# Kernel optimization log

Hardware: AMD Instinct MI355X
Metric: run time of the kernel (lower is better)

The kernel has to match this reference:

```python
import jax, jax.numpy as jnp
import numpy as np

B, T, D, H = 2, 4096, 1024, 16
DK, DV, C = 64, 128, 64  # head_k_dim, head_v_dim, chunk size


def setup_inputs() -> dict:
    key = jax.random.key(0)
    ks = jax.random.split(key, 7)
    std = 0.02
    return {
        "x": jax.random.normal(ks[0], (B, T, D), jnp.float32),
        "Wq": jax.random.normal(ks[1], (D, D), jnp.float32) * std,
        "Wk": jax.random.normal(ks[2], (D, D), jnp.float32) * std,
        "Wv": jax.random.normal(ks[3], (D, 2 * D), jnp.float32) * std,
        "Wg": jax.random.normal(ks[4], (D, 2 * D), jnp.float32) * std,
        "Wo": jax.random.normal(ks[5], (2 * D, D), jnp.float32) * std,
        "g_norm_w": jnp.ones((DV,), jnp.float32),
    }


def _rope(q, k):  # q,k: [B,T,H,DK], neox-style rotate-half rotary
    dk = q.shape[-1]
    inv = 1.0 / (10000.0 ** (jnp.arange(0, dk, 2, dtype=jnp.float32) / dk))
    t = jnp.arange(q.shape[1], dtype=jnp.float32)
    f = t[:, None] * inv[None, :]                      # [T, dk/2]
    cos = jnp.cos(f)[None, :, None, :]
    sin = jnp.sin(f)[None, :, None, :]
    def rot(x):
        x1, x2 = jnp.split(x, 2, axis=-1)
        return jnp.concatenate([x1 * cos - x2 * sin, x1 * sin + x2 * cos], -1)
    return rot(q), rot(k)


def reference(x, Wq, Wk, Wv, Wg, Wo, g_norm_w):
    b, t, _ = x.shape
    nc = t // C
    q = (x @ Wq).reshape(b, t, H, DK)
    k = (x @ Wk).reshape(b, t, H, DK)
    v = (x @ Wv).reshape(b, t, H, DV)
    g = (x @ Wg).reshape(b, t, H, DV)
    q, k = _rope(q, k)
    q = q * (DK ** -0.5)

    # per-head retention decay: gamma_h = 1 - 2^(-5-h)
    gamma = 1.0 - jnp.exp2(-5.0 - jnp.arange(H, dtype=jnp.float32))  # [H]
    i = jnp.arange(C, dtype=jnp.float32)
    dq = gamma[:, None] ** (i + 1.0)          # [H,C] cross-chunk decay on q
    dkv = gamma[:, None] ** (C - 1.0 - i)     # [H,C] decay of k into state
    rel = i[:, None] - i[None, :]
    Dmat = jnp.where(rel >= 0, gamma[:, None, None] ** jnp.maximum(rel, 0.0), 0.0)  # [H,C,C]
    gC = gamma ** C

    to_chunks = lambda a: a.reshape(b, nc, C, H, a.shape[-1]).transpose(1, 0, 3, 2, 4)
    qc, kc, vc = to_chunks(q), to_chunks(k), to_chunks(v)  # [NC,B,H,C,d]

    def step(S, inp):
        qi, ki, vi = inp
        o_inter = jnp.einsum('bhcd,bhde->bhce', qi * dq[None, :, :, None], S)
        A = jnp.einsum('bhid,bhjd->bhij', qi, ki) * Dmat[None]
        o_intra = jnp.einsum('bhij,bhje->bhie', A, vi)
        S = gC[None, :, None, None] * S + jnp.einsum('bhjd,bhje->bhde', ki * dkv[None, :, :, None], vi)
        return S, o_inter + o_intra

    S0 = jnp.zeros((b, H, DK, DV), x.dtype)
    _, o = jax.lax.scan(step, S0, (qc, kc, vc))            # [NC,B,H,C,DV]
    o = o.transpose(1, 0, 3, 2, 4).reshape(b, t, H, DV)

    # fused per-head RMSNorm + swish gate
    rms = o * jax.lax.rsqrt(jnp.mean(o * o, axis=-1, keepdims=True) + 1e-5) * g_norm_w
    o = rms * (g * jax.nn.sigmoid(g))
    return o.reshape(b, t, H * DV) @ Wo
```

## Files before the change

kernel.cpp:

```cpp
#include <hip/hip_runtime.h>
#include <stdint.h>
#include <type_traits>

typedef unsigned short u16;
typedef __attribute__((ext_vector_type(8))) short short8;
typedef __attribute__((ext_vector_type(4))) float f32x4;

#define MFMA16(a,b,c) __builtin_amdgcn_mfma_f32_16x16x32_bf16(a,b,c,0,0,0)

__device__ __forceinline__ u16 f2bf(float f){
  uint32_t u = __builtin_bit_cast(uint32_t, f);
  u += 0x7FFFu + ((u>>16)&1u);
  return (u16)(u>>16);
}
__device__ __forceinline__ float bf2f(u16 h){
  uint32_t u = ((uint32_t)h)<<16;
  return __builtin_bit_cast(float, u);
}

__global__ __launch_bounds__(256) void prep(const float* __restrict__ x, u16* __restrict__ xb,
    const float* __restrict__ Wq, const float* __restrict__ Wk, const float* __restrict__ Wv,
    const float* __restrict__ Wg, const float* __restrict__ Wo,
    u16* __restrict__ WcatT, u16* __restrict__ WoT){
  int bid = blockIdx.x;
  if (bid < 8192){
    int i = (bid*256 + threadIdx.x)*4;
    float4 v = *(const float4*)&x[i];
    uint2 u;
    u.x = (uint32_t)f2bf(v.x) | ((uint32_t)f2bf(v.y)<<16);
    u.y = (uint32_t)f2bf(v.z) | ((uint32_t)f2bf(v.w)<<16);
    *(uint2*)&xb[i] = u;
    return;
  }
  bid -= 8192;
  const float* src; u16* dst; int R, Cc, tc, tr;
  if (bid < 1024){        src=Wq; dst=WcatT;             R=1024; Cc=1024; int b=bid;      tc=(b&31)*32; tr=(b>>5)*32; }
  else if (bid < 2048){   src=Wk; dst=WcatT+1024*1024;   R=1024; Cc=1024; int b=bid-1024; tc=(b&31)*32; tr=(b>>5)*32; }
  else if (bid < 4096){   src=Wv; dst=WcatT+2048*1024;   R=1024; Cc=2048; int b=bid-2048; tc=(b&63)*32; tr=(b>>6)*32; }
  else if (bid < 6144){   src=Wg; dst=WcatT+4096*1024;   R=1024; Cc=2048; int b=bid-4096; tc=(b&63)*32; tr=(b>>6)*32; }
  else {                  src=Wo; dst=WoT;               R=2048; Cc=1024; int b=bid-6144; tc=(b&31)*32; tr=(b>>5)*32; }
  __shared__ float tile[32][33];
  int lr = threadIdx.x>>5, lc = threadIdx.x&31;
  #pragma unroll
  for (int p=0;p<4;p++)
    tile[lr+p*8][lc] = src[(size_t)(tr+lr+p*8)*Cc + tc + lc];
  __syncthreads();
  #pragma unroll
  for (int p=0;p<4;p++)
    dst[(size_t)(tc+lr+p*8)*R + tr + lc] = f2bf(tile[lc][lr+p*8]);
}

__global__ __launch_bounds__(512,1) void gemm1_256(const u16* __restrict__ A,
    const u16* __restrict__ BT, u16* __restrict__ C){
  __shared__ u16 L[4*16384];
  const int flat = blockIdx.y*24 + blockIdx.x;
  const int xcd  = flat & 7, loc = flat >> 3;
  const int bm   = xcd*4 + (loc & 3);
  const int bn   = loc >> 2;
  const int t = threadIdx.x;
  const int w = t>>6, l = t&63;
  const int wm = w>>2, wn = w&3;
  const int lr = l&15, lg = l>>4;
  const int srow = t>>2;
  const int gsw = ((t&3) - (t>>3)) & 3;
  const size_t aoff = (size_t)(bm*256 + srow)*1024 + gsw*8;
  const size_t boff = (size_t)(bn*256 + srow)*1024 + gsw*8;
  const int sdo = t*8;

  u16 *p0 = L, *p1 = L+16384, *p2 = L+32768, *p3 = L+49152;

  auto STAGE = [&](u16* buf, int k0){
    __builtin_amdgcn_global_load_lds(&A[aoff + k0],                     buf + sdo,               16,0,0);
    __builtin_amdgcn_global_load_lds(&A[aoff + (size_t)128*1024 + k0],  buf + sdo + 4096,        16,0,0);
    __builtin_amdgcn_global_load_lds(&BT[boff + k0],                    buf + 8192 + sdo,        16,0,0);
    __builtin_amdgcn_global_load_lds(&BT[boff + (size_t)128*1024 + k0], buf + 8192 + sdo + 4096, 16,0,0);
  };
  auto LDA = [&](const u16* base, int row)->short8 {
    return *(const short8*)(base + row*32 + (((lg + (row>>1))&3)<<3));
  };

  f32x4 acc[8][4];
  #pragma unroll
  for (int m=0;m<8;m++)
    #pragma unroll
    for (int n=0;n<4;n++) acc[m][n] = (f32x4){0.f,0.f,0.f,0.f};

  STAGE(p0, 0); STAGE(p1, 32); STAGE(p2, 64);
  asm volatile("s_waitcnt vmcnt(8)" ::: "memory");
  __builtin_amdgcn_s_barrier();
  short8 afA[4], afB[4], bf4[4], bf4n[4];
  #pragma unroll
  for (int m=0;m<4;m++) afA[m] = LDA(p0, wm*128 + m*16 + lr);
  #pragma unroll
  for (int n=0;n<4;n++) bf4[n] = LDA(p0 + 8192, wn*64 + n*16 + lr);

  for (int kt=0; kt<32; ++kt){
    #pragma unroll
    for (int m=0;m<4;m++) afB[m] = LDA(p0, wm*128 + (m+4)*16 + lr);
    if (kt+3 < 32) STAGE(p3, (kt+3)*32);
    __builtin_amdgcn_s_setprio(1);
    #pragma unroll
    for (int m=0;m<4;m++)
      #pragma unroll
      for (int n=0;n<4;n++)
        acc[m][n] = MFMA16(afA[m], bf4[n], acc[m][n]);
    __builtin_amdgcn_s_setprio(0);
    asm volatile("s_waitcnt lgkmcnt(0)" ::: "memory");
    __builtin_amdgcn_sched_barrier(0);
    if      (kt < 29)  asm volatile("s_waitcnt vmcnt(8)" ::: "memory");
    else if (kt == 29) asm volatile("s_waitcnt vmcnt(4)" ::: "memory");
    else               asm volatile("s_waitcnt vmcnt(0)" ::: "memory");
    __builtin_amdgcn_s_barrier();
    __builtin_amdgcn_sched_barrier(0);
    if (kt+1 < 32){
      #pragma unroll
      for (int m=0;m<4;m++) afA[m]  = LDA(p1, wm*128 + m*16 + lr);
      #pragma unroll
      for (int n=0;n<4;n++) bf4n[n] = LDA(p1 + 8192, wn*64 + n*16 + lr);
    }
    __builtin_amdgcn_s_setprio(1);
    #pragma unroll
    for (int m=0;m<4;m++)
      #pragma unroll
      for (int n=0;n<4;n++)
        acc[m+4][n] = MFMA16(afB[m], bf4[n], acc[m+4][n]);
    __builtin_amdgcn_s_setprio(0);
    if (kt+1 < 32){
      #pragma unroll
      for (int n=0;n<4;n++) bf4[n] = bf4n[n];
    }
    { u16* tp=p0; p0=p1; p1=p2; p2=p3; p3=tp; }
  }

  __syncthreads();
  const bool qk = (bn < 8);
  const float qscale = (bn < 4) ? 0.125f : 1.0f;
  #pragma unroll
  for (int s=0;s<4;++s){
    if (wm == (s>>1)){
      #pragma unroll
      for (int mm=0;mm<4;++mm){
        const int m = (s&1)*4 + mm;
        if (qk){
          #pragma unroll
          for (int n=0;n<2;n++){
            float inv = exp2f((float)(n*16+lr) * (-13.287712379549449f/32.0f));
            #pragma unroll
            for (int r=0;r<4;r++){
              int grow = bm*256 + wm*128 + m*16 + lg*4 + r;
              float f = (float)(grow & 4095) * inv;
              float sn, cs; __sincosf(f, &sn, &cs);
              float x1 = acc[m][n][r], x2 = acc[m][n+2][r];
              int lrow = mm*16 + lg*4 + r;
              L[lrow*264 + wn*64 + n*16 + lr]     = f2bf((x1*cs - x2*sn)*qscale);
              L[lrow*264 + wn*64 + (n+2)*16 + lr] = f2bf((x1*sn + x2*cs)*qscale);
            }
          }
        } else {
          #pragma unroll
          for (int n=0;n<4;n++)
            #pragma unroll
            for (int r=0;r<4;r++)
              L[(mm*16+lg*4+r)*264 + wn*64 + n*16 + lr] = f2bf(acc[m][n][r]);
        }
      }
    }
    __syncthreads();
    #pragma unroll
    for (int p=0;p<4;p++){
      int idx = p*512 + t;
      int row = idx>>5, gr = idx&31;
      *(short8*)&C[(size_t)(bm*256 + s*64 + row)*6144 + bn*256 + gr*8] =
        *(const short8*)&L[row*264 + gr*8];
    }
    __syncthreads();
  }
}

__global__ __launch_bounds__(256) void gemm2_nt(const u16* __restrict__ A,
    const u16* __restrict__ BT, float* __restrict__ C, int M, int N, int K){
  __shared__ u16 L[3*8192];
  const int flat = blockIdx.y*gridDim.x + blockIdx.x;
  const int xcd  = flat & 7, loc = flat >> 3;
  const int bm   = xcd*8 + (loc & 7);
  const int bn   = loc >> 3;
  const int t = threadIdx.x;
  const int w = t>>6, l = t&63;
  const int wr = (w>>1)*64, wc = (w&1)*64;
  const int lr = l&15, lg = l>>4;
  const int srow = t>>2;
  const int gsw  = ((t&3) - (t>>3)) & 3;
  const int scol = gsw*8;
  const size_t aoff = (size_t)(bm*128 + srow)*K + scol;
  const size_t boff = (size_t)(bn*128 + srow)*K + scol;
  const int sdo = t*8;

  u16 *a0 = L,          *b0 = L + 4096;
  u16 *a1 = L + 8192,   *b1 = L + 12288;
  u16 *a2 = L + 16384,  *b2 = L + 20480;

  auto STAGE = [&](u16* la, u16* lb, int k0){
    __builtin_amdgcn_global_load_lds(&A[aoff + k0],                 la + sdo,        16, 0, 0);
    __builtin_amdgcn_global_load_lds(&A[aoff + (size_t)64*K + k0],  la + sdo + 2048, 16, 0, 0);
    __builtin_amdgcn_global_load_lds(&BT[boff + k0],                lb + sdo,        16, 0, 0);
    __builtin_amdgcn_global_load_lds(&BT[boff + (size_t)64*K + k0], lb + sdo + 2048, 16, 0, 0);
  };
  auto LDR = [&](const u16* base, int row)->short8 {
    return *(const short8*)(base + row*32 + (((lg + (row>>1))&3)<<3));
  };

  f32x4 acc[4][4];
  for (int m=0;m<4;m++) for (int n=0;n<4;n++) acc[m][n] = (f32x4){0.f,0.f,0.f,0.f};

  const int NT = K >> 5;
  STAGE(a0, b0, 0);
  STAGE(a1, b1, 32);
  asm volatile("s_waitcnt vmcnt(4)" ::: "memory");
  __builtin_amdgcn_s_barrier();
  short8 af01[2], af23[2], bfr[4], bfrn[4];
  #pragma unroll
  for (int m=0;m<2;m++) af01[m] = LDR(a0, wr + m*16 + lr);
  #pragma unroll
  for (int n=0;n<4;n++) bfr[n] = LDR(b0, wc + n*16 + lr);

  for (int kt=0; kt<NT; ++kt){
    #pragma unroll
    for (int m=0;m<2;m++) af23[m] = LDR(a0, wr + (m+2)*16 + lr);
    if (kt+2 < NT) STAGE(a2, b2, (kt+2)*32);
    __builtin_amdgcn_s_setprio(1);
    #pragma unroll
    for (int m=0;m<2;m++)
      #pragma unroll
      for (int n=0;n<4;n++)
        acc[m][n] = MFMA16(af01[m], bfr[n], acc[m][n]);
    __builtin_amdgcn_s_setprio(0);
    asm volatile("s_waitcnt lgkmcnt(0)" ::: "memory");
    __builtin_amdgcn_sched_barrier(0);
    if (kt < NT-2) asm volatile("s_waitcnt vmcnt(4)" ::: "memory");
    else           asm volatile("s_waitcnt vmcnt(0)" ::: "memory");
    __builtin_amdgcn_s_barrier();
    __builtin_amdgcn_sched_barrier(0);
    if (kt+1 < NT){
      #pragma unroll
      for (int m=0;m<2;m++) af01[m] = LDR(a1, wr + m*16 + lr);
      #pragma unroll
      for (int n=0;n<4;n++) bfrn[n] = LDR(b1, wc + n*16 + lr);
    }
    __builtin_amdgcn_s_setprio(1);
    #pragma unroll
    for (int m=0;m<2;m++)
      #pragma unroll
      for (int n=0;n<4;n++)
        acc[m+2][n] = MFMA16(af23[m], bfr[n], acc[m+2][n]);
    __builtin_amdgcn_s_setprio(0);
    if (kt+1 < NT){
      #pragma unroll
      for (int n=0;n<4;n++) bfr[n] = bfrn[n];
    }
    { u16* tp=a0; a0=a1; a1=a2; a2=tp; }
    { u16* tp=b0; b0=b1; b1=b2; b2=tp; }
  }

  #pragma unroll
  for (int m=0;m<4;m++)
    #pragma unroll
    for (int n=0;n<4;n++){
    int row = bm*128 + wr + m*16 + lg*4;
    int col = bn*128 + wc + n*16 + lr;
    #pragma unroll
    for (int r=0;r<4;r++)
      C[(size_t)(row+r)*N + col] = acc[m][n][r];
  }
}

__global__ __launch_bounds__(256) void retention_r1(const u16* __restrict__ qkvg,
    u16* __restrict__ o, u16* __restrict__ states){
  int bid = blockIdx.x;
  int c = bid & 63, h = (bid>>6)&15, b = bid>>10;
  int t = threadIdx.x, w = t>>6, l = t&63, lr = l&15, lg = l>>4;
  __shared__ u16 SH[17280];
  __shared__ float pw[72];
  u16* kT    = SH;
  u16* vT    = SH + 4096;
  u16* A_lds = SH + 12288;
  float log2g = log2f(1.0f - exp2f(-5.0f - (float)h));
  if (t < 65) pw[t] = exp2f(log2g*(float)t);
  const size_t rowbase = (size_t)(b*4096 + c*64);
  __syncthreads();

  {
    int rp = t>>3, cg = t&7;
    int r0 = rp*2;
    short8 k0v = *(const short8*)&qkvg[(rowbase+r0  )*6144 + 1024 + h*64 + cg*8];
    short8 k1v = *(const short8*)&qkvg[(rowbase+r0+1)*6144 + 1024 + h*64 + cg*8];
    float d0 = pw[63-r0], d1 = pw[62-r0];
    #pragma unroll
    for (int j=0;j<8;j++){
      int d = cg*8+j;
      uint32_t pk = (uint32_t)f2bf(bf2f((u16)k0v[j])*d0) | ((uint32_t)f2bf(bf2f((u16)k1v[j])*d1)<<16);
      *(uint32_t*)&kT[d*64 + (((r0>>3) ^ (d>>3))<<3) + (r0&7)] = pk;
    }
    #pragma unroll
    for (int p=0;p<2;p++){
      int it = t + p*256;
      int vrp = it>>4, vcg = it&15;
      int vr0 = vrp*2;
      short8 v0 = *(const short8*)&qkvg[(rowbase+vr0  )*6144 + 2048 + h*128 + vcg*8];
      short8 v1 = *(const short8*)&qkvg[(rowbase+vr0+1)*6144 + 2048 + h*128 + vcg*8];
      #pragma unroll
      for (int j=0;j<8;j++){
        int e = vcg*8+j;
        uint32_t pv = (uint32_t)(u16)v0[j] | ((uint32_t)(u16)v1[j]<<16);
        *(uint32_t*)&vT[e*64 + (((vr0>>3) ^ ((e>>3)&7))<<3) + (vr0&7)] = pv;
      }
    }
  }

  f32x4 z4 = {0.f,0.f,0.f,0.f};
  f32x4 accA[4] = {z4,z4,z4,z4};
  #pragma unroll
  for (int ks=0;ks<2;ks++){
    short8 aq = *(const short8*)&qkvg[(rowbase + w*16+lr)*6144 + h*64 + ks*32 + lg*8];
    #pragma unroll
    for (int n=0;n<4;n++){
      short8 bk = *(const short8*)&qkvg[(rowbase + n*16+lr)*6144 + 1024 + h*64 + ks*32 + lg*8];
      accA[n] = MFMA16(aq, bk, accA[n]);
    }
  }
  #pragma unroll
  for (int n=0;n<4;n++)
    #pragma unroll
    for (int r=0;r<4;r++){
    int i = w*16 + lg*4 + r, j = n*16 + lr;
    float v = (i>=j) ? accA[n][r]*pw[i-j] : 0.0f;
    A_lds[i*72 + j] = f2bf(v);
  }
  __syncthreads();

  f32x4 accO[8], accS[8];
  #pragma unroll
  for (int n=0;n<8;n++){ accO[n]=z4; accS[n]=z4; }
  #pragma unroll
  for (int ks=0;ks<2;ks++){
    int rk = w*16+lr;
    short8 aA = *(const short8*)&A_lds[rk*72 + ks*32+lg*8];
    short8 aK = *(const short8*)&kT[rk*64 + (((ks*4+lg) ^ (rk>>3))<<3)];
    #pragma unroll
    for (int n=0;n<8;n++){
      int e2 = n*16+lr;
      short8 bv = *(const short8*)&vT[e2*64 + (((ks*4+lg) ^ ((e2>>3)&7))<<3)];
      accO[n] = MFMA16(aA, bv, accO[n]);
      accS[n] = MFMA16(aK, bv, accS[n]);
    }
  }

  __syncthreads();
  u16* oB = SH;
  u16* sB = SH + 8448;
  #pragma unroll
  for (int n=0;n<8;n++)
    #pragma unroll
    for (int r=0;r<4;r++){
    int i = w*16 + lg*4 + r, e = n*16 + lr;
    oB[i*132 + e] = f2bf(accO[n][r]);
    sB[e*68 + i]  = f2bf(accS[n][r]);
  }
  __syncthreads();
  const size_t ob = rowbase*2048 + h*128;
  const size_t sb = ((size_t)(b*16+h)*64 + c)*8192;
  {
    int orow = t>>2, ocol = (t&3)*32;
    #pragma unroll
    for (int q=0;q<4;q++)
      *(short8*)&o[ob + (size_t)orow*2048 + ocol + q*8] = *(const short8*)&oB[orow*132 + ocol + q*8];
    int se = t>>1, sd = (t&1)*32;
    #pragma unroll
    for (int q=0;q<4;q++)
      *(short8*)&states[sb + (size_t)se*64 + sd + q*8] = *(const short8*)&sB[se*68 + sd + q*8];
  }
}

__global__ __launch_bounds__(256) void retention_r2(const u16* __restrict__ qkvg,
    const u16* __restrict__ states, u16* __restrict__ o){
  int bid = blockIdx.x;
  int xq = bid & 7, qq = bid >> 3;
  int bh = xq*4 + (qq & 3);
  int vblk = qq >> 2;
  int h = bh & 15, b = bh >> 4;
  int t = threadIdx.x, w = t>>6, l = t&63, lr = l&15, lg = l>>4;
  int e0 = vblk*16;
  float log2g = log2f(1.0f - exp2f(-5.0f - (float)h));
  float gC = exp2f(64.0f*log2g);
  float dqv[4];
  #pragma unroll
  for (int r=0;r<4;r++) dqv[r] = exp2f(log2g*(float)(w*16 + lg*4 + r + 1));
  float st[16];
  #pragma unroll
  for (int i=0;i<16;i++) st[i]=0.f;
  const size_t sbase = ((size_t)(b*16+h)*64)*8192 + (size_t)(e0+lr)*64 + lg*8;
  const size_t qb = (size_t)(b*4096)*6144 + h*64 + (size_t)(w*16+lr)*6144 + lg*8;
  const size_t obh = (size_t)(b*4096)*2048 + h*128 + e0 + lr;
  short8 nsc0 = *(const short8*)&states[sbase];
  short8 nsc1 = *(const short8*)&states[sbase + 32];
  short8 naq0 = *(const short8*)&qkvg[qb];
  short8 naq1 = *(const short8*)&qkvg[qb + 32];
  for (int c=0;c<64;c++){
    short8 sc0 = nsc0, sc1 = nsc1, aq0 = naq0, aq1 = naq1;
    if (c < 63){
      nsc0 = *(const short8*)&states[sbase + (size_t)(c+1)*8192];
      nsc1 = *(const short8*)&states[sbase + (size_t)(c+1)*8192 + 32];
      naq0 = *(const short8*)&qkvg[qb + (size_t)(c+1)*64*6144];
      naq1 = *(const short8*)&qkvg[qb + (size_t)(c+1)*64*6144 + 32];
    }
    f32x4 acc = {0.f,0.f,0.f,0.f};
    short8 bs0, bs1;
    #pragma unroll
    for (int dd=0;dd<8;dd++) bs0[dd] = (short)f2bf(st[dd]);
    #pragma unroll
    for (int dd=0;dd<8;dd++) bs1[dd] = (short)f2bf(st[dd+8]);
    acc = MFMA16(aq0, bs0, acc);
    acc = MFMA16(aq1, bs1, acc);
    #pragma unroll
    for (int r=0;r<4;r++){
      int i = w*16 + lg*4 + r;
      size_t oi = obh + (size_t)(c*64 + i)*2048;
      o[oi] = f2bf(bf2f(o[oi]) + dqv[r]*acc[r]);
    }
    #pragma unroll
    for (int i2=0;i2<8;i2++) st[i2]   = gC*st[i2]   + bf2f((u16)sc0[i2]);
    #pragma unroll
    for (int i2=0;i2<8;i2++) st[i2+8] = gC*st[i2+8] + bf2f((u16)sc1[i2]);
  }
}

__global__ __launch_bounds__(256) void norm_gate(const u16* __restrict__ o,
    const u16* __restrict__ qkvg, const float* __restrict__ gnw, u16* __restrict__ og){
  int g16 = threadIdx.x >> 4;
  int l16 = threadIdx.x & 15;
  int rowh = blockIdx.x*16 + g16;
  int row = rowh >> 4, h = rowh & 15;
  short8 vv = *(const short8*)(o + (size_t)row*2048 + h*128 + l16*8);
  float v[8];
  float ss = 0.f;
  #pragma unroll
  for (int j=0;j<8;j++){ v[j] = bf2f((u16)vv[j]); ss += v[j]*v[j]; }
  #pragma unroll
  for (int off=8; off; off>>=1) ss += __shfl_xor(ss, off);
  float rs = rsqrtf(ss*(1.0f/128.0f) + 1e-5f);
  short8 gg = *(const short8*)(qkvg + (size_t)row*6144 + 4096 + h*128 + l16*8);
  float4 w0 = *(const float4*)&gnw[l16*8];
  float4 w1 = *(const float4*)&gnw[l16*8 + 4];
  float wv[8] = {w0.x,w0.y,w0.z,w0.w,w1.x,w1.y,w1.z,w1.w};
  short8 res;
  #pragma unroll
  for (int j=0;j<8;j++){
    float gj = bf2f((u16)gg[j]);
    float rj = v[j]*rs*wv[j] * (gj/(1.f+expf(-gj)));
    res[j] = (short)f2bf(rj);
  }
  *(short8*)(og + (size_t)row*2048 + h*128 + l16*8) = res;
}

extern "C" void kernel_launch(void* const* d_in, const int* in_sizes, int n_in,
                              void* d_out, int out_size, void* d_ws, size_t ws_size,
                              hipStream_t stream){
  const float* x   = (const float*)d_in[0];
  const float* Wq  = (const float*)d_in[1];
  const float* Wk  = (const float*)d_in[2];
  const float* Wv  = (const float*)d_in[3];
  const float* Wg  = (const float*)d_in[4];
  const float* Wo  = (const float*)d_in[5];
  const float* gnw = (const float*)d_in[6];
  float* out = (float*)d_out;

  const size_t NEED = 171966464ull;
  if (ws_size < NEED) return;

  char* base = (char*)d_ws;
  u16* qkvg  = (u16*)(base);
  u16* obuf  = (u16*)(base + 100663296);
  u16* WoT   = (u16*)(base + 134217728);
  u16* xb    = (u16*)(base + 138412032);
  u16* WcatT = (u16*)(base + 155189248);
  u16* stt   = (u16*)(base + 138412032);
  u16* og    = (u16*)(base + 138412032);

  prep<<<16384,256,0,stream>>>(x, xb, Wq, Wk, Wv, Wg, Wo, WcatT, WoT);
  gemm1_256<<<dim3(24,32),512,0,stream>>>(xb, WcatT, qkvg);
  retention_r1<<<2048,256,0,stream>>>(qkvg, obuf, stt);
  retention_r2<<<256,256,0,stream>>>(qkvg, stt, obuf);
  norm_gate<<<8192,256,0,stream>>>(obuf, qkvg, gnw, og);
  gemm2_nt<<<dim3(8,64),256,0,stream>>>(og, WoT, out, 8192, 1024, 2048);
}
```

Baseline: 283.2 us.

## Switch projection GEMM to double-buffered BK=64 stages with full-K fragment preload

Replaces the four-slot, one-barrier-per-32-K pipeline in the fused QKVG projection GEMM with two 64-wide K buffers. Each iteration loads fragments for both 32-K halves and issues one 64-K stage ahead. This halves the barrier and loop count and gives 32 MFMAs per half. In exchange, prefetch depth drops from three stages to one and the loop waits on vmcnt(0) every iteration, so global-load latency may be less hidden. Fragment register pressure also rises.

```diff
diff --git a/kernel.cpp b/kernel.cpp
--- a/kernel.cpp
+++ b/kernel.cpp
@@ -52,7 +52,7 @@
 
 __global__ __launch_bounds__(512,1) void gemm1_256(const u16* __restrict__ A,
     const u16* __restrict__ BT, u16* __restrict__ C){
-  __shared__ u16 L[4*16384];
+  __shared__ u16 L[2*32768];
   const int flat = blockIdx.y*24 + blockIdx.x;
   const int xcd  = flat & 7, loc = flat >> 3;
   const int bm   = xcd*4 + (loc & 3);
@@ -67,13 +67,16 @@
   const size_t boff = (size_t)(bn*256 + srow)*1024 + gsw*8;
   const int sdo = t*8;
 
-  u16 *p0 = L, *p1 = L+16384, *p2 = L+32768, *p3 = L+49152;
+  u16 *cur = L, *oth = L + 32768;
 
   auto STAGE = [&](u16* buf, int k0){
-    __builtin_amdgcn_global_load_lds(&A[aoff + k0],                     buf + sdo,               16,0,0);
-    __builtin_amdgcn_global_load_lds(&A[aoff + (size_t)128*1024 + k0],  buf + sdo + 4096,        16,0,0);
-    __builtin_amdgcn_global_load_lds(&BT[boff + k0],                    buf + 8192 + sdo,        16,0,0);
-    __builtin_amdgcn_global_load_lds(&BT[boff + (size_t)128*1024 + k0], buf + 8192 + sdo + 4096, 16,0,0);
+    #pragma unroll
+    for (int ks=0; ks<2; ++ks){
+      __builtin_amdgcn_global_load_lds(&A[aoff + k0 + ks*32],                     buf + ks*8192 + sdo,               16,0,0);
+      __builtin_amdgcn_global_load_lds(&A[aoff + (size_t)128*1024 + k0 + ks*32],  buf + ks*8192 + sdo + 4096,        16,0,0);
+      __builtin_amdgcn_global_load_lds(&BT[boff + k0 + ks*32],                    buf + 16384 + ks*8192 + sdo,        16,0,0);
+      __builtin_amdgcn_global_load_lds(&BT[boff + (size_t)128*1024 + k0 + ks*32], buf + 16384 + ks*8192 + sdo + 4096, 16,0,0);
+    }
   };
   auto LDA = [&](const u16* base, int row)->short8 {
     return *(const short8*)(base + row*32 + (((lg + (row>>1))&3)<<3));
@@ -85,51 +88,47 @@
     #pragma unroll
     for (int n=0;n<4;n++) acc[m][n] = (f32x4){0.f,0.f,0.f,0.f};
 
-  STAGE(p0, 0); STAGE(p1, 32); STAGE(p2, 64);
-  asm volatile("s_waitcnt vmcnt(8)" ::: "memory");
+  STAGE(cur, 0);
+  asm volatile("s_waitcnt vmcnt(0)" ::: "memory");
   __builtin_amdgcn_s_barrier();
-  short8 afA[4], afB[4], bf4[4], bf4n[4];
-  #pragma unroll
-  for (int m=0;m<4;m++) afA[m] = LDA(p0, wm*128 + m*16 + lr);
-  #pragma unroll
-  for (int n=0;n<4;n++) bf4[n] = LDA(p0 + 8192, wn*64 + n*16 + lr);
-
-  for (int kt=0; kt<32; ++kt){
-    #pragma unroll
-    for (int m=0;m<4;m++) afB[m] = LDA(p0, wm*128 + (m+4)*16 + lr);
-    if (kt+3 < 32) STAGE(p3, (kt+3)*32);
+  short8 f0A[8], f0B[4], f1A[8], f1B[4];
+  #pragma unroll
+  for (int m=0;m<8;m++) f0A[m] = LDA(cur, wm*128 + m*16 + lr);
+  #pragma unroll
+  for (int n=0;n<4;n++) f0B[n] = LDA(cur + 16384, wn*64 + n*16 + lr);
+
+  for (int kt=0; kt<16; ++kt){
+    #pragma unroll
+    for (int m=0;m<8;m++) f1A[m] = LDA(cur + 8192, wm*128 + m*16 + lr);
+    #pragma unroll
+    for (int n=0;n<4;n++) f1B[n] = LDA(cur + 16384 + 8192, wn*64 + n*16 + lr);
+    if (kt+1 < 16) STAGE(oth, (kt+1)*64);
     __builtin_amdgcn_s_setprio(1);
     #pragma unroll
-    for (int m=0;m<4;m++)
+    for (int m=0;m<8;m++)
       #pragma unroll
       for (int n=0;n<4;n++)
-        acc[m][n] = MFMA16(afA[m], bf4[n], acc[m][n]);
+        acc[m][n] = MFMA16(f0A[m], f0B[n], acc[m][n]);
     __builtin_amdgcn_s_setprio(0);
     asm volatile("s_waitcnt lgkmcnt(0)" ::: "memory");
     __builtin_amdgcn_sched_barrier(0);
-    if      (kt < 29)  asm volatile("s_waitcnt vmcnt(8)" ::: "memory");
-    else if (kt == 29) asm volatile("s_waitcnt vmcnt(4)" ::: "memory");
-    else               asm volatile("s_waitcnt vmcnt(0)" ::: "memory");
+    asm volatile("s_waitcnt vmcnt(0)" ::: "memory");
     __builtin_amdgcn_s_barrier();
     __builtin_amdgcn_sched_barrier(0);
-    if (kt+1 < 32){
-      #pragma unroll
-      for (int m=0;m<4;m++) afA[m]  = LDA(p1, wm*128 + m*16 + lr);
-      #pragma unroll
-      for (int n=0;n<4;n++) bf4n[n] = LDA(p1 + 8192, wn*64 + n*16 + lr);
+    if (kt+1 < 16){
+      #pragma unroll
+      for (int m=0;m<8;m++) f0A[m] = LDA(oth, wm*128 + m*16 + lr);
+      #pragma unroll
+      for (int n=0;n<4;n++) f0B[n] = LDA(oth + 16384, wn*64 + n*16 + lr);
     }
     __builtin_amdgcn_s_setprio(1);
     #pragma unroll
-    for (int m=0;m<4;m++)
+    for (int m=0;m<8;m++)
       #pragma unroll
       for (int n=0;n<4;n++)
-        acc[m+4][n] = MFMA16(afB[m], bf4[n], acc[m+4][n]);
+        acc[m][n] = MFMA16(f1A[m], f1B[n], acc[m][n]);
     __builtin_amdgcn_s_setprio(0);
-    if (kt+1 < 32){
-      #pragma unroll
-      for (int n=0;n<4;n++) bf4[n] = bf4n[n];
-    }
-    { u16* tp=p0; p0=p1; p1=p2; p2=p3; p3=tp; }
+    { u16* tp=cur; cur=oth; oth=tp; }
   }
 
   __syncthreads();
```

Result: no change. 284.4 us (+0.4%).
